# Kernel optimization log

Measured on AMD Instinct MI355X. Metric: run time of the kernel, lower is better.

The kernel has to match this reference:

```python
import jax, jax.numpy as jnp
import numpy as np

H = 32          # query heads
HKV = 8         # kv heads
HD = 128        # head dim
BS = 64         # sparse block size
LOCAL = 16      # local blocks
VERT = 8        # vertical stride
STEP = 1        # head sliding step = max(1, VERT // H) for non-homo heads
BASE = 1000000.0
ROPE_SCALE = 1.0
SCALE = 1.0 / np.sqrt(HD)


def setup_inputs() -> dict:
    key = jax.random.key(0)
    ks = jax.random.split(key, 6)
    T, D = 2048, H * HD
    std = 0.02
    return {
        'hidden_states': jax.random.normal(ks[0], (T, D), jnp.float32),
        'positions': jnp.arange(T, dtype=jnp.int32),
        'Wq': jax.random.normal(ks[1], (D, H * HD), jnp.float32) * std,
        'bq': jnp.zeros((H * HD,), jnp.float32),
        'Wk': jax.random.normal(ks[2], (D, HKV * HD), jnp.float32) * std,
        'bk': jnp.zeros((HKV * HD,), jnp.float32),
        'Wv': jax.random.normal(ks[3], (D, HKV * HD), jnp.float32) * std,
        'bv': jnp.zeros((HKV * HD,), jnp.float32),
        'Wo': jax.random.normal(ks[4], (D, D), jnp.float32) * std,
        'bo': jnp.zeros((D,), jnp.float32),
    }


def _rope_cos_sin(positions):
    # neox-style rotary, linear scaling (factor 1.0 -> identity)
    inv_freq = 1.0 / (BASE ** (jnp.arange(0, HD, 2, dtype=jnp.float32) / HD))  # [HD/2]
    t = positions.astype(jnp.float32) / ROPE_SCALE                             # [T]
    freqs = t[:, None] * inv_freq[None, :]                                     # [T, HD/2]
    return jnp.cos(freqs), jnp.sin(freqs)


def _apply_rope(x, cos, sin):
    # x: [T, h, HD], neox: rotate halves
    x1, x2 = x[..., : HD // 2], x[..., HD // 2 :]
    c, s = cos[:, None, :], sin[:, None, :]
    return jnp.concatenate([x1 * c - x2 * s, x2 * c + x1 * s], axis=-1)


def _block_sparse_mask(T):
    # per-head local + vertical-stride block pattern, causal at token level
    blk = jnp.arange(T) // BS
    qb, kb = blk[:, None], blk[None, :]                      # [T,T] block ids
    heads = jnp.arange(H)
    local = (qb - kb) < LOCAL                                # [T,T]
    vert = ((kb[None, :, :] + heads[:, None, None] * STEP + 1) % VERT) == 0  # [H,T,T]
    causal = jnp.arange(T)[:, None] >= jnp.arange(T)[None, :]
    return causal[None] & (local[None] | vert)               # [H,T,T] bool


def reference(hidden_states, positions, Wq, bq, Wk, bk, Wv, bv, Wo, bo):
    T = hidden_states.shape[0]
    q = (hidden_states @ Wq + bq).reshape(T, H, HD)
    k = (hidden_states @ Wk + bk).reshape(T, HKV, HD)
    v = (hidden_states @ Wv + bv).reshape(T, HKV, HD)

    cos, sin = _rope_cos_sin(positions)
    q = _apply_rope(q, cos, sin)
    k = _apply_rope(k, cos, sin)

    # GQA: repeat kv heads to match query heads
    k = jnp.repeat(k, H // HKV, axis=1)   # [T,H,HD]
    v = jnp.repeat(v, H // HKV, axis=1)

    scores = jnp.einsum('shd,thd->hst', q, k) * SCALE         # [H,T,T]
    mask = _block_sparse_mask(T)
    scores = jnp.where(mask, scores, jnp.finfo(scores.dtype).min)
    probs = jax.nn.softmax(scores, axis=-1)
    out = jnp.einsum('hst,thd->shd', probs, v).reshape(T, H * HD)
    return out @ Wo + bo
```

## Files before the change

kernel.cpp:

```cpp
#include <hip/hip_runtime.h>
#include <type_traits>

#define H_    32
#define HKV_  8
#define HD_   128
#define D_    4096
#define KVD_  1024
#define NQKV_ 6144

typedef __attribute__((ext_vector_type(8))) short s8v;
typedef __attribute__((ext_vector_type(4))) float f4v;

__device__ __forceinline__ float b2f(unsigned short u) {
  union { unsigned int i; float f; } v; v.i = ((unsigned int)u) << 16; return v.f;
}
__device__ __forceinline__ unsigned short f2b(float f) {
  unsigned int u = __float_as_uint(f);
  u += 0x7fffu + ((u >> 16) & 1u);
  return (unsigned short)(u >> 16);
}

__device__ __forceinline__ void gload16(const unsigned short* g, unsigned short* l) {
  __builtin_amdgcn_global_load_lds((const __attribute__((address_space(1))) void*)g,
                                   (__attribute__((address_space(3))) void*)l, 16, 0, 0);
}

__global__ void cvt_bf16(const float* __restrict__ x, unsigned short* __restrict__ y,
                         int n8)
{
  int i = blockIdx.x * blockDim.x + threadIdx.x;
  if (i >= n8) return;
  const float4* xp = (const float4*)x + (size_t)i * 2;
  float4 a = xp[0], b = xp[1];
  s8v v;
  v[0] = (short)f2b(a.x); v[1] = (short)f2b(a.y);
  v[2] = (short)f2b(a.z); v[3] = (short)f2b(a.w);
  v[4] = (short)f2b(b.x); v[5] = (short)f2b(b.y);
  v[6] = (short)f2b(b.z); v[7] = (short)f2b(b.w);
  *(s8v*)(y + (size_t)i * 8) = v;
}

__global__ void concat_bias(const float* __restrict__ bq, const float* __restrict__ bk,
                            const float* __restrict__ bv, float* __restrict__ o)
{
  int i = blockIdx.x * blockDim.x + threadIdx.x;
  float v = (i < D_) ? bq[i] : (i < D_ + KVD_) ? bk[i - D_] : bv[i - D_ - KVD_];
  o[i] = v;
}

__global__ __launch_bounds__(256) void cvt_transpose(
    const float* __restrict__ W, unsigned short* __restrict__ Wt, int K, int N)
{
  __shared__ unsigned short tile[64][72];
  const int k0 = blockIdx.y * 64, n0 = blockIdx.x * 64;
  const int tid = threadIdx.x;
#pragma unroll
  for (int it = 0; it < 4; ++it) {
    int idx = tid + it * 256;
    int r = idx >> 4;
    int c = (idx & 15) << 2;
    float4 w = *(const float4*)(W + (size_t)(k0 + r) * N + n0 + c);
    tile[c + 0][r] = f2b(w.x); tile[c + 1][r] = f2b(w.y);
    tile[c + 2][r] = f2b(w.z); tile[c + 3][r] = f2b(w.w);
  }
  __syncthreads();
#pragma unroll
  for (int it = 0; it < 2; ++it) {
    int idx = tid + it * 256;
    int n = idx >> 3;
    int kk = (idx & 7) << 3;
    *(s8v*)(Wt + (size_t)(n0 + n) * K + k0 + kk) = *(const s8v*)&tile[n][kk];
  }
}

__global__ __launch_bounds__(256) void vtrans(
    const unsigned short* __restrict__ S, int lds_, unsigned short* __restrict__ Dst,
    int T)
{
  __shared__ unsigned short tile[64][72];
  const int v0 = blockIdx.x * 64, t0 = blockIdx.y * 64;
  const int tid = threadIdx.x;
#pragma unroll
  for (int it = 0; it < 2; ++it) {
    int idx = tid + it * 256;
    int tr = idx >> 3;
    int vc = (idx & 7) << 3;
    s8v val = *(const s8v*)(S + (size_t)(t0 + tr) * lds_ + v0 + vc);
#pragma unroll
    for (int u = 0; u < 8; ++u) tile[vc + u][tr] = (unsigned short)val[u];
  }
  __syncthreads();
#pragma unroll
  for (int it = 0; it < 2; ++it) {
    int idx = tid + it * 256;
    int vr = idx >> 3;
    int tc = (idx & 7) << 3;
    *(s8v*)(Dst + (size_t)(v0 + vr) * T + t0 + tc) = *(const s8v*)&tile[vr][tc];
  }
}

template <typename OT>
__global__ __launch_bounds__(512, 2) void gemm_bt4p(
    const unsigned short* __restrict__ A, const unsigned short* __restrict__ Bt,
    const float* __restrict__ bias, OT* __restrict__ C,
    int M, int N, int K, int ldc)
{
  __shared__ __align__(16) unsigned short lds[65536];

  const int tid  = threadIdx.x;
  const int wave = tid >> 6;
  const int lane = tid & 63;
  const int l16  = lane & 15;
  const int quad = lane >> 4;
  const int wm   = wave >> 2;
  const int wn   = wave & 3;

  const int nbx = N >> 8;
  const int nwg = nbx * (M >> 8);
  int bid = blockIdx.x;
  if ((nwg & 7) == 0) bid = (bid & 7) * (nwg >> 3) + (bid >> 3);
  const int row0 = (bid / nbx) << 8;
  const int col0 = (bid % nbx) << 8;

  const int srow = lane >> 2;
  const int scol = (((lane & 3) ^ ((lane >> 3) & 3)) << 3);
  const unsigned short* ApL = A  + (size_t)(row0 + wave * 32 + srow) * K + scol;
  const unsigned short* BpL = Bt + (size_t)(col0 + wave * 32 + srow) * K + scol;

  unsigned short* ldsA = lds;
  unsigned short* ldsB = lds + 32768;
  const int wst = wave * 1024;

  const int sl = ((quad ^ ((l16 >> 1) & 3)) << 3);
  const int arow = wm * 128 + l16;
  const int brow = wn * 64 + l16;

  f4v acc[8][4] = {};
  const int nt = K >> 6;

  {
    const unsigned short* sa = ApL;
    const unsigned short* sb = BpL;
    gload16(sa,                       ldsA + wst);
    gload16(sa + 16 * (size_t)K,      ldsA + wst + 512);
    gload16(sb,                       ldsB + wst);
    gload16(sb + 16 * (size_t)K,      ldsB + wst + 512);
    gload16(sa + 32,                  ldsA + 8192 + wst);
    gload16(sa + 32 + 16 * (size_t)K, ldsA + 8192 + wst + 512);
    gload16(sb + 32,                  ldsB + 8192 + wst);
    gload16(sb + 32 + 16 * (size_t)K, ldsB + 8192 + wst + 512);
  }
  asm volatile("s_waitcnt vmcnt(4)" ::: "memory");
  asm volatile("s_barrier" ::: "memory");

  for (int t = 0; t < nt; ++t) {
    const int p = t & 1;
    const unsigned short* Ab0 = ldsA + p * 16384;
    const unsigned short* Ab1 = Ab0 + 8192;
    const unsigned short* Bb0 = ldsB + p * 16384;
    const unsigned short* Bb1 = Bb0 + 8192;
    unsigned short* An = ldsA + (p ^ 1) * 16384;
    unsigned short* Bn = ldsB + (p ^ 1) * 16384;
    const bool pre = (t + 1 < nt);
    const unsigned short* sa = ApL + (size_t)(t + 1) * 64;
    const unsigned short* sb = BpL + (size_t)(t + 1) * 64;

    s8v a[8], b0, b1, b2, b3;

    b0 = *(const s8v*)&Bb0[(brow +  0) * 32 + sl];
    b1 = *(const s8v*)&Bb0[(brow + 16) * 32 + sl];
#pragma unroll
    for (int i = 0; i < 8; ++i)
      a[i] = *(const s8v*)&Ab0[(arow + i * 16) * 32 + sl];
    if (pre) {
      gload16(sa,                  An + wst);
      gload16(sa + 16 * (size_t)K, An + wst + 512);
    }
    __builtin_amdgcn_s_setprio(1);
#pragma unroll
    for (int i = 0; i < 8; ++i) {
      acc[i][0] = __builtin_amdgcn_mfma_f32_16x16x32_bf16(a[i], b0, acc[i][0], 0, 0, 0);
      acc[i][1] = __builtin_amdgcn_mfma_f32_16x16x32_bf16(a[i], b1, acc[i][1], 0, 0, 0);
    }
    __builtin_amdgcn_s_setprio(0);

    b2 = *(const s8v*)&Bb0[(brow + 32) * 32 + sl];
    b3 = *(const s8v*)&Bb0[(brow + 48) * 32 + sl];
    if (pre) {
      gload16(sb,                  Bn + wst);
      gload16(sb + 16 * (size_t)K, Bn + wst + 512);
      asm volatile("s_waitcnt vmcnt(4)" ::: "memory");
    } else {
      asm volatile("s_waitcnt vmcnt(0)" ::: "memory");
    }
    asm volatile("s_barrier" ::: "memory");
    __builtin_amdgcn_s_setprio(1);
#pragma unroll
    for (int i = 0; i < 8; ++i) {
      acc[i][2] = __builtin_amdgcn_mfma_f32_16x16x32_bf16(a[i], b2, acc[i][2], 0, 0, 0);
      acc[i][3] = __builtin_amdgcn_mfma_f32_16x16x32_bf16(a[i], b3, acc[i][3], 0, 0, 0);
    }
    __builtin_amdgcn_s_setprio(0);

    b2 = *(const s8v*)&Bb1[(brow + 32) * 32 + sl];
    b3 = *(const s8v*)&Bb1[(brow + 48) * 32 + sl];
#pragma unroll
    for (int i = 0; i < 8; ++i)
      a[i] = *(const s8v*)&Ab1[(arow + i * 16) * 32 + sl];
    if (pre) {
      gload16(sa + 32,                  An + 8192 + wst);
      gload16(sa + 32 + 16 * (size_t)K, An + 8192 + wst + 512);
    }
    __builtin_amdgcn_s_setprio(1);
#pragma unroll
    for (int i = 0; i < 8; ++i) {
      acc[i][2] = __builtin_amdgcn_mfma_f32_16x16x32_bf16(a[i], b2, acc[i][2], 0, 0, 0);
      acc[i][3] = __builtin_amdgcn_mfma_f32_16x16x32_bf16(a[i], b3, acc[i][3], 0, 0, 0);
    }
    __builtin_amdgcn_s_setprio(0);

    b0 = *(const s8v*)&Bb1[(brow +  0) * 32 + sl];
    b1 = *(const s8v*)&Bb1[(brow + 16) * 32 + sl];
    if (pre) {
      gload16(sb + 32,                  Bn + 8192 + wst);
      gload16(sb + 32 + 16 * (size_t)K, Bn + 8192 + wst + 512);
      asm volatile("s_waitcnt vmcnt(4)" ::: "memory");
    }
    asm volatile("s_barrier" ::: "memory");
    __builtin_amdgcn_s_setprio(1);
#pragma unroll
    for (int i = 0; i < 8; ++i) {
      acc[i][0] = __builtin_amdgcn_mfma_f32_16x16x32_bf16(a[i], b0, acc[i][0], 0, 0, 0);
      acc[i][1] = __builtin_amdgcn_mfma_f32_16x16x32_bf16(a[i], b1, acc[i][1], 0, 0, 0);
    }
    __builtin_amdgcn_s_setprio(0);
  }

#pragma unroll
  for (int j = 0; j < 4; ++j) {
    const int col = col0 + wn * 64 + j * 16 + l16;
    const float bc = bias[col];
#pragma unroll
    for (int i = 0; i < 8; ++i) {
      const int rowb = row0 + wm * 128 + i * 16 + quad * 4;
#pragma unroll
      for (int r = 0; r < 4; ++r) {
        float o = acc[i][j][r] + bc;
        if constexpr (std::is_same_v<OT, float>) C[(size_t)(rowb + r) * ldc + col] = o;
        else                                     C[(size_t)(rowb + r) * ldc + col] = f2b(o);
      }
    }
  }
}

__global__ __launch_bounds__(512, 1) void gemm_on(
    const unsigned short* __restrict__ A, const unsigned short* __restrict__ Bt,
    const float* __restrict__ bias, float* __restrict__ C,
    int M, int N, int K)
{
  __shared__ __align__(16) unsigned short lds[49152];

  const int tid  = threadIdx.x;
  const int wave = tid >> 6;
  const int lane = tid & 63;
  const int l16  = lane & 15;
  const int quad = lane >> 4;
  const int wm   = wave >> 2;
  const int wn   = wave & 3;

  const int nbx = N >> 7;
  const int nwg = nbx * (M >> 8);
  int bid = blockIdx.x;
  if ((nwg & 7) == 0) bid = (bid & 7) * (nwg >> 3) + (bid >> 3);
  const int row0 = (bid / nbx) << 8;
  const int col0 = (bid % nbx) << 7;

  const int srow = lane >> 2;
  const int scol = (((lane & 3) ^ ((lane >> 3) & 3)) << 3);
  const unsigned short* ApL = A  + (size_t)(row0 + wave * 32 + srow) * K + scol;
  const unsigned short* BpL = Bt + (size_t)(col0 + wave * 16 + srow) * K + scol;

  unsigned short* ldsA = lds;
  unsigned short* ldsB = lds + 32768;
  const int wstA = wave * 1024;
  const int wstB = wave * 512;

  const int sl = ((quad ^ ((l16 >> 1) & 3)) << 3);
  const int arow = wm * 128 + l16;
  const int brow = wn * 32 + l16;

  f4v acc[8][2] = {};
  const int nt = K >> 6;

  gload16(ApL,                       ldsA + wstA);
  gload16(ApL + 16 * (size_t)K,      ldsA + wstA + 512);
  gload16(BpL,                       ldsB + wstB);
  gload16(ApL + 32,                  ldsA + 8192 + wstA);
  gload16(ApL + 32 + 16 * (size_t)K, ldsA + 8192 + wstA + 512);
  gload16(BpL + 32,                  ldsB + 4096 + wstB);
  asm volatile("s_waitcnt vmcnt(3)" ::: "memory");
  asm volatile("s_barrier" ::: "memory");

  for (int t = 0; t < nt; ++t) {
    const int p = t & 1;
    const unsigned short* Ab0 = ldsA + p * 16384;
    const unsigned short* Ab1 = Ab0 + 8192;
    const unsigned short* Bb0 = ldsB + p * 8192;
    const unsigned short* Bb1 = Bb0 + 4096;
    unsigned short* An = ldsA + (p ^ 1) * 16384;
    unsigned short* Bn = ldsB + (p ^ 1) * 8192;
    const bool pre = (t + 1 < nt);
    const unsigned short* sa = ApL + (size_t)(t + 1) * 64;
    const unsigned short* sb = BpL + (size_t)(t + 1) * 64;

    s8v a[8], b0, b1;

    b0 = *(const s8v*)&Bb0[(brow +  0) * 32 + sl];
    b1 = *(const s8v*)&Bb0[(brow + 16) * 32 + sl];
#pragma unroll
    for (int i = 0; i < 8; ++i)
      a[i] = *(const s8v*)&Ab0[(arow + i * 16) * 32 + sl];
    if (pre) {
      gload16(sa,                  An + wstA);
      gload16(sa + 16 * (size_t)K, An + wstA + 512);
      gload16(sb,                  Bn + wstB);
    }
    __builtin_amdgcn_s_setprio(1);
#pragma unroll
    for (int i = 0; i < 8; ++i) {
      acc[i][0] = __builtin_amdgcn_mfma_f32_16x16x32_bf16(a[i], b0, acc[i][0], 0, 0, 0);
      acc[i][1] = __builtin_amdgcn_mfma_f32_16x16x32_bf16(a[i], b1, acc[i][1], 0, 0, 0);
    }
    __builtin_amdgcn_s_setprio(0);
    if (pre) { asm volatile("s_waitcnt vmcnt(3)" ::: "memory"); }
    else     { asm volatile("s_waitcnt vmcnt(0)" ::: "memory"); }
    asm volatile("s_barrier" ::: "memory");

    b0 = *(const s8v*)&Bb1[(brow +  0) * 32 + sl];
    b1 = *(const s8v*)&Bb1[(brow + 16) * 32 + sl];
#pragma unroll
    for (int i = 0; i < 8; ++i)
      a[i] = *(const s8v*)&Ab1[(arow + i * 16) * 32 + sl];
    if (pre) {
      gload16(sa + 32,                  An + 8192 + wstA);
      gload16(sa + 32 + 16 * (size_t)K, An + 8192 + wstA + 512);
      gload16(sb + 32,                  Bn + 4096 + wstB);
    }
    __builtin_amdgcn_s_setprio(1);
#pragma unroll
    for (int i = 0; i < 8; ++i) {
      acc[i][0] = __builtin_amdgcn_mfma_f32_16x16x32_bf16(a[i], b0, acc[i][0], 0, 0, 0);
      acc[i][1] = __builtin_amdgcn_mfma_f32_16x16x32_bf16(a[i], b1, acc[i][1], 0, 0, 0);
    }
    __builtin_amdgcn_s_setprio(0);
    if (pre) { asm volatile("s_waitcnt vmcnt(3)" ::: "memory"); }
    asm volatile("s_barrier" ::: "memory");
  }

#pragma unroll
  for (int j = 0; j < 2; ++j) {
    const int col = col0 + wn * 32 + j * 16 + l16;
    const float bc = bias[col];
#pragma unroll
    for (int i = 0; i < 8; ++i) {
      const int rowb = row0 + wm * 128 + i * 16 + quad * 4;
#pragma unroll
      for (int r = 0; r < 4; ++r)
        C[(size_t)(rowb + r) * N + col] = acc[i][j][r] + bc;
    }
  }
}

__global__ void sincos_tab(const int* __restrict__ pos, float* __restrict__ ct,
                           float* __restrict__ st)
{
  const int t = blockIdx.x, d = threadIdx.x;
  float inv = powf(1.0e6f, -(float)d * (1.0f / 64.0f));
  float fr  = (float)pos[t] * inv;
  float s, c;
  sincosf(fr, &s, &c);
  ct[t * 64 + d] = c;
  st[t * 64 + d] = s;
}

__global__ __launch_bounds__(320) void rope_apply2(
    unsigned short* __restrict__ qkv,
    const float* __restrict__ ct, const float* __restrict__ st, int T)
{
  const int t   = blockIdx.x;
  const int tid = threadIdx.x;
  const int hh  = tid >> 3;
  const int d0  = (tid & 7) << 3;
  unsigned short* p = qkv + (size_t)t * NQKV_ + hh * HD_;
  const float g = (hh < H_) ? (0.08838834764831845f * 1.4426950408889634f) : 1.0f;

  s8v x1 = *(const s8v*)(p + d0);
  s8v x2 = *(const s8v*)(p + 64 + d0);
  const float4* cp = (const float4*)(ct + t * 64 + d0);
  const float4* sp = (const float4*)(st + t * 64 + d0);
  float4 ca = cp[0], cb = cp[1], sa = sp[0], sb = sp[1];
  float cc[8] = {ca.x, ca.y, ca.z, ca.w, cb.x, cb.y, cb.z, cb.w};
  float ss[8] = {sa.x, sa.y, sa.z, sa.w, sb.x, sb.y, sb.z, sb.w};

  s8v o1, o2;
#pragma unroll
  for (int u = 0; u < 8; ++u) {
    float a = b2f((unsigned short)x1[u]);
    float b = b2f((unsigned short)x2[u]);
    o1[u] = (short)f2b((a * cc[u] - b * ss[u]) * g);
    o2[u] = (short)f2b((b * cc[u] + a * ss[u]) * g);
  }
  *(s8v*)(p + d0)      = o1;
  *(s8v*)(p + 64 + d0) = o2;
}

__global__ __launch_bounds__(256) void attn_sparse(
    const unsigned short* __restrict__ QKV, int ldq,
    const unsigned short* __restrict__ Vt, unsigned short* __restrict__ O, int T)
{
  __shared__ __align__(16) unsigned short lds[16384];
  unsigned short* ldsK = lds;
  unsigned short* ldsV = lds + 8192;
  unsigned short* ldsP = lds;

  const int h    = blockIdx.x;
  const int qb   = (gridDim.y - 1) - blockIdx.y;
  const int hkv  = h >> 2;
  const int tid  = threadIdx.x;
  const int wave = tid >> 6;
  const int lane = tid & 63;
  const int l16  = lane & 15;
  const int quad = lane >> 4;

  const int qrow = qb * 64 + wave * 16 + l16;
  s8v qf[4];
#pragma unroll
  for (int s = 0; s < 4; ++s)
    qf[s] = *(const s8v*)(QKV + (size_t)qrow * ldq + h * HD_ + s * 32 + quad * 8);

  const int lr4 = lane >> 2;
  const int lc8 = (lane & 3) << 3;
  const unsigned short* Kp0 = QKV + (size_t)(wave * 16 + lr4) * ldq
                              + D_ + hkv * HD_ + lc8;
  unsigned short* Kd0 = ldsK + wave * 512;
  const unsigned short* Vp0 = Vt + (size_t)(hkv * HD_ + wave * 32 + lr4) * T + lc8;
  unsigned short* Vd0 = ldsV + wave * 1024;

  float mrow[4] = {-1e30f, -1e30f, -1e30f, -1e30f};
  float lrow[4] = {0.f, 0.f, 0.f, 0.f};
  f4v oacc[8] = {};
  const int rowinb = wave * 16 + quad * 4;

  for (int kb = 0; kb <= qb; ++kb) {
    if (!((qb - kb < 16) || (((kb + h + 1) & 7) == 0))) continue;

    __syncthreads();
    {
      const unsigned short* kp = Kp0 + (size_t)(kb * 64) * ldq;
      const unsigned short* vp = Vp0 + kb * 64;
#pragma unroll
      for (int t = 0; t < 4; ++t)
        gload16(kp + t * 32, Kd0 + t * 2048);
#pragma unroll
      for (int t = 0; t < 4; ++t)
        gload16(vp + (size_t)((t >> 1) * 16) * T + (t & 1) * 32,
                Vd0 + (t & 1) * 4096 + (t >> 1) * 512);
    }
    __syncthreads();

    f4v sacc[4] = {};
#pragma unroll
    for (int kt = 0; kt < 4; ++kt) {
#pragma unroll
      for (int s = 0; s < 4; ++s) {
        s8v b = *(const s8v*)&ldsK[s * 2048 + (kt * 16 + l16) * 32 + quad * 8];
        sacc[kt] = __builtin_amdgcn_mfma_f32_16x16x32_bf16(qf[s], b, sacc[kt], 0, 0, 0);
      }
    }
    __syncthreads();

    const bool diag = (kb == qb);
    float p[4][4];
#pragma unroll
    for (int r = 0; r < 4; ++r) {
      float mx = -1e30f;
#pragma unroll
      for (int kt = 0; kt < 4; ++kt) {
        float sc = sacc[kt][r];
        if (diag && (kt * 16 + l16 > rowinb + r)) sc = -1e30f;
        p[r][kt] = sc;
        mx = fmaxf(mx, sc);
      }
#pragma unroll
      for (int off = 1; off < 16; off <<= 1)
        mx = fmaxf(mx, __shfl_xor(mx, off));
      float newm = fmaxf(mrow[r], mx);
      float alpha = exp2f(mrow[r] - newm);
      mrow[r] = newm;
      float rs = 0.f;
#pragma unroll
      for (int kt = 0; kt < 4; ++kt) {
        unsigned short pb = f2b(exp2f(p[r][kt] - newm));
        ldsP[wave * 1152 + (quad * 4 + r) * 72 + kt * 16 + l16] = pb;
        rs += b2f(pb);
      }
#pragma unroll
      for (int off = 1; off < 16; off <<= 1)
        rs += __shfl_xor(rs, off);
      lrow[r] = lrow[r] * alpha + rs;
#pragma unroll
      for (int dt = 0; dt < 8; ++dt) oacc[dt][r] *= alpha;
    }

#pragma unroll
    for (int s2 = 0; s2 < 2; ++s2) {
      s8v af = *(const s8v*)&ldsP[wave * 1152 + l16 * 72 + s2 * 32 + quad * 8];
#pragma unroll
      for (int dt = 0; dt < 8; ++dt) {
        s8v vf = *(const s8v*)&ldsV[s2 * 4096 + (dt * 16 + l16) * 32 + quad * 8];
        oacc[dt] = __builtin_amdgcn_mfma_f32_16x16x32_bf16(af, vf, oacc[dt], 0, 0, 0);
      }
    }
  }

#pragma unroll
  for (int r = 0; r < 4; ++r) {
    float inv = 1.0f / lrow[r];
    size_t rowoff = (size_t)(qb * 64 + rowinb + r) * D_ + h * HD_;
#pragma unroll
    for (int dt = 0; dt < 8; ++dt)
      O[rowoff + dt * 16 + l16] = f2b(oacc[dt][r] * inv);
  }
}

extern "C" void kernel_launch(void* const* d_in, const int* in_sizes, int n_in,
                              void* d_out, int out_size, void* d_ws, size_t ws_size,
                              hipStream_t stream)
{
  const float* hs  = (const float*)d_in[0];
  const int*   pos = (const int*)d_in[1];
  const float* Wq  = (const float*)d_in[2];
  const float* bq  = (const float*)d_in[3];
  const float* Wk  = (const float*)d_in[4];
  const float* bk  = (const float*)d_in[5];
  const float* Wv  = (const float*)d_in[6];
  const float* bv  = (const float*)d_in[7];
  const float* Wo  = (const float*)d_in[8];
  const float* bo  = (const float*)d_in[9];
  float* out = (float*)d_out;

  const int T = in_sizes[1];

  const size_t nQ = (size_t)T * D_;
  unsigned short* hsb  = (unsigned short*)d_ws;
  unsigned short* qkv  = hsb + nQ;
  unsigned short* vt   = qkv + (size_t)T * NQKV_;
  unsigned short* wbuf = vt  + (size_t)KVD_ * T;
  unsigned short* tail = wbuf + (size_t)NQKV_ * D_;
  float* bqkv = (float*)tail;
  float* ct   = bqkv + NQKV_;
  float* st   = ct + (size_t)T * 64;
  unsigned short* abuf = hsb;

  dim3 blk(256);
  cvt_bf16<<<dim3((int)(nQ / 8 / 256)), blk, 0, stream>>>(hs, hsb, (int)(nQ / 8));
  concat_bias<<<dim3(NQKV_ / 256), blk, 0, stream>>>(bq, bk, bv, bqkv);
  sincos_tab<<<dim3(T), dim3(64), 0, stream>>>(pos, ct, st);

  cvt_transpose<<<dim3(D_ / 64,   D_ / 64), blk, 0, stream>>>(Wq, wbuf, D_, D_);
  cvt_transpose<<<dim3(KVD_ / 64, D_ / 64), blk, 0, stream>>>(
      Wk, wbuf + (size_t)D_ * D_, D_, KVD_);
  cvt_transpose<<<dim3(KVD_ / 64, D_ / 64), blk, 0, stream>>>(
      Wv, wbuf + (size_t)(D_ + KVD_) * D_, D_, KVD_);

  gemm_bt4p<unsigned short><<<dim3((NQKV_ / 256) * (T / 256)), dim3(512), 0, stream>>>(
      hsb, wbuf, bqkv, qkv, T, NQKV_, D_, NQKV_);

  rope_apply2<<<dim3(T), dim3(320), 0, stream>>>(qkv, ct, st, T);
  vtrans<<<dim3(KVD_ / 64, T / 64), blk, 0, stream>>>(
      qkv + D_ + KVD_, NQKV_, vt, T);

  attn_sparse<<<dim3(H_, T / 64), blk, 0, stream>>>(qkv, NQKV_, vt, abuf, T);

  cvt_transpose<<<dim3(D_ / 64, D_ / 64), blk, 0, stream>>>(Wo, wbuf, D_, D_);
  gemm_on<<<dim3((D_ / 128) * (T / 256)), dim3(512), 0, stream>>>(
      abuf, wbuf, bo, out, T, D_, D_);
}
```

Before: 495.8 us.

## Rework QKV GEMM to 4 waves with 128x128 per-wave output tiles

The QKV projection GEMM goes from 8 waves with 128x64 sub-tiles per wave to 4 waves with 128x128 sub-tiles per wave, still on a 256x256 block tile. Each wave now loads 8 A and 8 B fragments per k-substep and issues 64 MFMAs, which raises operand reuse from registers and halves the barrier phases per k-step. The cost is 256 accumulator floats per lane, so register pressure is high and spills are possible. Only one 256-thread block fits per CU, which reduces latency hiding.

```diff
diff --git a/kernel.cpp b/kernel.cpp
--- a/kernel.cpp
+++ b/kernel.cpp
@@ -99,10 +99,9 @@
   }
 }
 
-template <typename OT>
-__global__ __launch_bounds__(512, 2) void gemm_bt4p(
+__global__ __launch_bounds__(256, 1) void gemm_w128(
     const unsigned short* __restrict__ A, const unsigned short* __restrict__ Bt,
-    const float* __restrict__ bias, OT* __restrict__ C,
+    const float* __restrict__ bias, unsigned short* __restrict__ C,
     int M, int N, int K, int ldc)
 {
   __shared__ __align__(16) unsigned short lds[65536];
@@ -112,8 +111,8 @@
   const int lane = tid & 63;
   const int l16  = lane & 15;
   const int quad = lane >> 4;
-  const int wm   = wave >> 2;
-  const int wn   = wave & 3;
+  const int wm   = wave >> 1;
+  const int wn   = wave & 1;
 
   const int nbx = N >> 8;
   const int nwg = nbx * (M >> 8);
@@ -124,33 +123,35 @@
 
   const int srow = lane >> 2;
   const int scol = (((lane & 3) ^ ((lane >> 3) & 3)) << 3);
-  const unsigned short* ApL = A  + (size_t)(row0 + wave * 32 + srow) * K + scol;
-  const unsigned short* BpL = Bt + (size_t)(col0 + wave * 32 + srow) * K + scol;
+  const unsigned short* ApL = A  + (size_t)(row0 + wave * 64 + srow) * K + scol;
+  const unsigned short* BpL = Bt + (size_t)(col0 + wave * 64 + srow) * K + scol;
 
   unsigned short* ldsA = lds;
   unsigned short* ldsB = lds + 32768;
-  const int wst = wave * 1024;
+  const int wst = wave * 2048;
 
   const int sl = ((quad ^ ((l16 >> 1) & 3)) << 3);
   const int arow = wm * 128 + l16;
-  const int brow = wn * 64 + l16;
-
-  f4v acc[8][4] = {};
+  const int brow = wn * 128 + l16;
+
+  f4v acc[8][8] = {};
   const int nt = K >> 6;
 
   {
-    const unsigned short* sa = ApL;
-    const unsigned short* sb = BpL;
-    gload16(sa,                       ldsA + wst);
-    gload16(sa + 16 * (size_t)K,      ldsA + wst + 512);
-    gload16(sb,                       ldsB + wst);
-    gload16(sb + 16 * (size_t)K,      ldsB + wst + 512);
-    gload16(sa + 32,                  ldsA + 8192 + wst);
-    gload16(sa + 32 + 16 * (size_t)K, ldsA + 8192 + wst + 512);
-    gload16(sb + 32,                  ldsB + 8192 + wst);
-    gload16(sb + 32 + 16 * (size_t)K, ldsB + 8192 + wst + 512);
-  }
-  asm volatile("s_waitcnt vmcnt(4)" ::: "memory");
+#pragma unroll
+    for (int u = 0; u < 4; ++u)
+      gload16(ApL + (size_t)(u * 16) * K,      ldsA + wst + u * 512);
+#pragma unroll
+    for (int u = 0; u < 4; ++u)
+      gload16(BpL + (size_t)(u * 16) * K,      ldsB + wst + u * 512);
+#pragma unroll
+    for (int u = 0; u < 4; ++u)
+      gload16(ApL + 32 + (size_t)(u * 16) * K, ldsA + 8192 + wst + u * 512);
+#pragma unroll
+    for (int u = 0; u < 4; ++u)
+      gload16(BpL + 32 + (size_t)(u * 16) * K, ldsB + 8192 + wst + u * 512);
+  }
+  asm volatile("s_waitcnt vmcnt(8)" ::: "memory");
   asm volatile("s_barrier" ::: "memory");
 
   for (int t = 0; t < nt; ++t) {
@@ -165,90 +166,68 @@
     const unsigned short* sa = ApL + (size_t)(t + 1) * 64;
     const unsigned short* sb = BpL + (size_t)(t + 1) * 64;
 
-    s8v a[8], b0, b1, b2, b3;
-
-    b0 = *(const s8v*)&Bb0[(brow +  0) * 32 + sl];
-    b1 = *(const s8v*)&Bb0[(brow + 16) * 32 + sl];
+    s8v a[8], b[8];
+
 #pragma unroll
     for (int i = 0; i < 8; ++i)
       a[i] = *(const s8v*)&Ab0[(arow + i * 16) * 32 + sl];
+#pragma unroll
+    for (int j = 0; j < 8; ++j)
+      b[j] = *(const s8v*)&Bb0[(brow + j * 16) * 32 + sl];
     if (pre) {
-      gload16(sa,                  An + wst);
-      gload16(sa + 16 * (size_t)K, An + wst + 512);
+#pragma unroll
+      for (int u = 0; u < 4; ++u)
+        gload16(sa + (size_t)(u * 16) * K, An + wst + u * 512);
+#pragma unroll
+      for (int u = 0; u < 4; ++u)
+        gload16(sb + (size_t)(u * 16) * K, Bn + wst + u * 512);
     }
     __builtin_amdgcn_s_setprio(1);
 #pragma unroll
-    for (int i = 0; i < 8; ++i) {
-      acc[i][0] = __builtin_amdgcn_mfma_f32_16x16x32_bf16(a[i], b0, acc[i][0], 0, 0, 0);
-      acc[i][1] = __builtin_amdgcn_mfma_f32_16x16x32_bf16(a[i], b1, acc[i][1], 0, 0, 0);
-    }
+    for (int i = 0; i < 8; ++i)
+#pragma unroll
+      for (int j = 0; j < 8; ++j)
+        acc[i][j] = __builtin_amdgcn_mfma_f32_16x16x32_bf16(a[i], b[j], acc[i][j], 0, 0, 0);
     __builtin_amdgcn_s_setprio(0);
-
-    b2 = *(const s8v*)&Bb0[(brow + 32) * 32 + sl];
-    b3 = *(const s8v*)&Bb0[(brow + 48) * 32 + sl];
-    if (pre) {
-      gload16(sb,                  Bn + wst);
-      gload16(sb + 16 * (size_t)K, Bn + wst + 512);
-      asm volatile("s_waitcnt vmcnt(4)" ::: "memory");
-    } else {
-      asm volatile("s_waitcnt vmcnt(0)" ::: "memory");
-    }
+    if (pre) { asm volatile("s_waitcnt vmcnt(8)" ::: "memory"); }
+    else     { asm volatile("s_waitcnt vmcnt(0)" ::: "memory"); }
     asm volatile("s_barrier" ::: "memory");
-    __builtin_amdgcn_s_setprio(1);
-#pragma unroll
-    for (int i = 0; i < 8; ++i) {
-      acc[i][2] = __builtin_amdgcn_mfma_f32_16x16x32_bf16(a[i], b2, acc[i][2], 0, 0, 0);
-      acc[i][3] = __builtin_amdgcn_mfma_f32_16x16x32_bf16(a[i], b3, acc[i][3], 0, 0, 0);
-    }
-    __builtin_amdgcn_s_setprio(0);
-
-    b2 = *(const s8v*)&Bb1[(brow + 32) * 32 + sl];
-    b3 = *(const s8v*)&Bb1[(brow + 48) * 32 + sl];
+
 #pragma unroll
     for (int i = 0; i < 8; ++i)
       a[i] = *(const s8v*)&Ab1[(arow + i * 16) * 32 + sl];
+#pragma unroll
+    for (int j = 0; j < 8; ++j)
+      b[j] = *(const s8v*)&Bb1[(brow + j * 16) * 32 + sl];
     if (pre) {
-      gload16(sa + 32,                  An + 8192 + wst);
-      gload16(sa + 32 + 16 * (size_t)K, An + 8192 + wst + 512);
+#pragma unroll
+      for (int u = 0; u < 4; ++u)
+        gload16(sa + 32 + (size_t)(u * 16) * K, An + 8192 + wst + u * 512);
+#pragma unroll
+      for (int u = 0; u < 4; ++u)
+        gload16(sb + 32 + (size_t)(u * 16) * K, Bn + 8192 + wst + u * 512);
     }
     __builtin_amdgcn_s_setprio(1);
 #pragma unroll
-    for (int i = 0; i < 8; ++i) {
-      acc[i][2] = __builtin_amdgcn_mfma_f32_16x16x32_bf16(a[i], b2, acc[i][2], 0, 0, 0);
-      acc[i][3] = __builtin_amdgcn_mfma_f32_16x16x32_bf16(a[i], b3, acc[i][3], 0, 0, 0);
-    }
+    for (int i = 0; i < 8; ++i)
+#pragma unroll
+      for (int j = 0; j < 8; ++j)
+        acc[i][j] = __builtin_amdgcn_mfma_f32_16x16x32_bf16(a[i], b[j], acc[i][j], 0, 0, 0);
     __builtin_amdgcn_s_setprio(0);
-
-    b0 = *(const s8v*)&Bb1[(brow +  0) * 32 + sl];
-    b1 = *(const s8v*)&Bb1[(brow + 16) * 32 + sl];
-    if (pre) {
-      gload16(sb + 32,                  Bn + 8192 + wst);
-      gload16(sb + 32 + 16 * (size_t)K, Bn + 8192 + wst + 512);
-      asm volatile("s_waitcnt vmcnt(4)" ::: "memory");
-    }
+    if (pre) { asm volatile("s_waitcnt vmcnt(8)" ::: "memory"); }
     asm volatile("s_barrier" ::: "memory");
-    __builtin_amdgcn_s_setprio(1);
-#pragma unroll
-    for (int i = 0; i < 8; ++i) {
-      acc[i][0] = __builtin_amdgcn_mfma_f32_16x16x32_bf16(a[i], b0, acc[i][0], 0, 0, 0);
-      acc[i][1] = __builtin_amdgcn_mfma_f32_16x16x32_bf16(a[i], b1, acc[i][1], 0, 0, 0);
-    }
-    __builtin_amdgcn_s_setprio(0);
-  }
-
-#pragma unroll
-  for (int j = 0; j < 4; ++j) {
-    const int col = col0 + wn * 64 + j * 16 + l16;
+  }
+
+#pragma unroll
+  for (int j = 0; j < 8; ++j) {
+    const int col = col0 + wn * 128 + j * 16 + l16;
     const float bc = bias[col];
 #pragma unroll
     for (int i = 0; i < 8; ++i) {
       const int rowb = row0 + wm * 128 + i * 16 + quad * 4;
 #pragma unroll
-      for (int r = 0; r < 4; ++r) {
-        float o = acc[i][j][r] + bc;
-        if constexpr (std::is_same_v<OT, float>) C[(size_t)(rowb + r) * ldc + col] = o;
-        else                                     C[(size_t)(rowb + r) * ldc + col] = f2b(o);
-      }
+      for (int r = 0; r < 4; ++r)
+        C[(size_t)(rowb + r) * ldc + col] = f2b(acc[i][j][r] + bc);
     }
   }
 }
@@ -573,7 +552,7 @@
   cvt_transpose<<<dim3(KVD_ / 64, D_ / 64), blk, 0, stream>>>(
       Wv, wbuf + (size_t)(D_ + KVD_) * D_, D_, KVD_);
 
-  gemm_bt4p<unsigned short><<<dim3((NQKV_ / 256) * (T / 256)), dim3(512), 0, stream>>>(
+  gemm_w128<<<dim3((NQKV_ / 256) * (T / 256)), dim3(256), 0, stream>>>(
       hsb, wbuf, bqkv, qkv, T, NQKV_, D_, NQKV_);
 
   rope_apply2<<<dim3(T), dim3(320), 0, stream>>>(qkv, ct, st, T);
```

Result: slower. 544.7 us (+9.8%).
